# Kernel optimization log

Measured on AMD Instinct MI355X. Metric: run time of the kernel, lower is better.

The kernel has to match this reference:

```python
import jax, jax.numpy as jnp
import numpy as np
import math

B, S, D, H = 1, 4096, 1024, 16
HD = D // H  # head_dim = 64


def setup_inputs() -> dict:
    key = jax.random.key(0)
    ks = jax.random.split(key, 6)
    x = jax.random.normal(ks[0], (B, S, D), dtype=jnp.float32)
    # Llama-style rotary frequencies: theta = 10000^{-2i/head_dim}
    inv_freq = 1.0 / (10000.0 ** (jnp.arange(0, HD, 2, dtype=jnp.float32) / HD))  # (HD/2,)
    t = jnp.arange(S, dtype=jnp.float32)
    freqs = jnp.outer(t, inv_freq)  # (S, HD/2)
    cos = jnp.cos(freqs)
    sin = jnp.sin(freqs)
    # additive causal mask (S, S): 0 on/below diagonal, -inf above
    mask = jnp.where(jnp.tril(jnp.ones((S, S), dtype=bool)), 0.0, -jnp.inf).astype(jnp.float32)
    scale = 1.0 / math.sqrt(D)
    wq = jax.random.normal(ks[1], (D, D), dtype=jnp.float32) * scale
    wk = jax.random.normal(ks[2], (D, D), dtype=jnp.float32) * scale
    wv = jax.random.normal(ks[3], (D, D), dtype=jnp.float32) * scale
    wo = jax.random.normal(ks[4], (D, D), dtype=jnp.float32) * scale
    return {"x": x, "cos": cos, "sin": sin, "mask": mask,
            "wq": wq, "wk": wk, "wv": wv, "wo": wo, "start_pos": 0}


def _rope(t, cos, sin):
    # t: (b, s, h, hd); cos/sin: (s, hd/2). Interleaved-pair complex rotation.
    b, s, h, hd = t.shape
    tr = t.reshape(b, s, h, hd // 2, 2)
    te, to = tr[..., 0], tr[..., 1]
    c = cos[None, :, None, :]
    sn = sin[None, :, None, :]
    oe = te * c - to * sn
    oo = te * sn + to * c
    return jnp.stack([oe, oo], axis=-1).reshape(b, s, h, hd)


def reference(x, cos, sin, mask, wq, wk, wv, wo, start_pos):
    b, s, d = x.shape
    h, hd = H, HD
    # Linear layers: y = x @ W.T (torch nn.Linear convention, W is (out,in))
    xq = (x @ wq.T).reshape(b, s, h, hd)
    xk = (x @ wk.T).reshape(b, s, h, hd)
    xv = (x @ wv.T).reshape(b, s, h, hd)
    xq = _rope(xq, cos, sin)
    xk = _rope(xk, cos, sin)
    # (b, h, s, hd)
    xq = xq.transpose(0, 2, 1, 3)
    xk = xk.transpose(0, 2, 1, 3)
    xv = xv.transpose(0, 2, 1, 3)
    scores = jnp.einsum('bhqd,bhkd->bhqk', xq, xk) / math.sqrt(hd)
    scores = scores + mask[None, None, :, :]
    attn = jax.nn.softmax(scores.astype(jnp.float32), axis=-1).astype(xq.dtype)
    out = jnp.einsum('bhqk,bhkd->bhqd', attn, xv)
    out = out.transpose(0, 2, 1, 3).reshape(b, s, d)
    return out @ wo.T
```

## Files before the change

### kernel.cpp

```cpp
#include <hip/hip_runtime.h>
#include <hip/hip_bf16.h>
#include <math.h>

typedef __bf16 bf16;
typedef __bf16 bf16x4 __attribute__((ext_vector_type(4)));
typedef __bf16 bf16x8 __attribute__((ext_vector_type(8)));
typedef float floatx4 __attribute__((ext_vector_type(4)));
typedef short short4v __attribute__((ext_vector_type(4)));

#define S_LEN 4096
#define DM 1024
#define NH 16
#define HD 64

#define GM 4096
#define GN 1024
#define GK 1024
#define FST 68

#define QSCALE 0.18033688011112042f

#define GLDS16(gp, lp) __builtin_amdgcn_global_load_lds( \
    (const __attribute__((address_space(1))) void*)(gp), \
    (__attribute__((address_space(3))) void*)(lp), 16, 0, 0)

__global__ void cvt_bf16(const float* __restrict__ x,  const float* __restrict__ wq,
                         const float* __restrict__ wk, const float* __restrict__ wv,
                         const float* __restrict__ wo, bf16* __restrict__ dst)
{
    size_t i4 = ((size_t)blockIdx.x * 256 + threadIdx.x) * 4;
    const float* src; size_t off;
    const size_t M1 = (size_t)1 << 20;
    if      (i4 < 4 * M1) { src = x;  off = i4;          }
    else if (i4 < 5 * M1) { src = wq; off = i4 - 4 * M1; }
    else if (i4 < 6 * M1) { src = wk; off = i4 - 5 * M1; }
    else if (i4 < 7 * M1) { src = wv; off = i4 - 6 * M1; }
    else                  { src = wo; off = i4 - 7 * M1; }
    float4 v = *(const float4*)(src + off);
    bf16x4 o = { (bf16)v.x, (bf16)v.y, (bf16)v.z, (bf16)v.w };
    *(bf16x4*)(&dst[i4]) = o;
}

__launch_bounds__(256)
__global__ void gemm_qkv(const bf16* __restrict__ A,
                         const bf16* __restrict__ B0, const bf16* __restrict__ B1,
                         const bf16* __restrict__ B2,
                         const float* __restrict__ cosp, const float* __restrict__ sinp,
                         bf16* __restrict__ Qw, bf16* __restrict__ Kw,
                         bf16* __restrict__ VTw)
{
    const int bid = blockIdx.x;
    const int swz = (bid & 7) * 192 + (bid >> 3);
    const int bz  = swz >> 9;
    const int rem = swz & 511;
    const int m0  = (rem >> 3) * 64;
    const int n0  = (rem & 7) * 128;
    const bf16* __restrict__ B = (bz == 0) ? B0 : (bz == 1 ? B1 : B2);

    const int tid  = threadIdx.x;
    const int wave = tid >> 6;
    const int lane = tid & 63;
    const int wm   = (wave >> 1) * 32;
    const int wn   = (wave & 1) * 64;
    const int lrow = lane >> 4;
    const int lcol = lane & 15;

    __shared__ __align__(16) bf16 As[64 * 64];
    __shared__ __align__(16) bf16 Bs[128 * 64];

    floatx4 acc[2][4];
    #pragma unroll
    for (int i = 0; i < 2; i++)
        #pragma unroll
        for (int j = 0; j < 4; j++) acc[i][j] = (floatx4){0.f, 0.f, 0.f, 0.f};

    const int swc = (((lane & 7) ^ ((lane >> 3) & 7))) * 8;
    const bf16* ga0 = A + (size_t)(m0 + wave * 16 + (lane >> 3)) * GK + swc;
    const bf16* gb0 = B + (size_t)(n0 + wave * 32 + (lane >> 3)) * GK + swc;
    bf16* la = &As[(wave * 16) * 64];
    bf16* lb = &Bs[(wave * 32) * 64];
    const int kof0 = ((0 + lrow) ^ (lcol & 7)) * 8;
    const int kof1 = ((4 + lrow) ^ (lcol & 7)) * 8;

    for (int kt = 0; kt < GK; kt += 64) {
        #pragma unroll
        for (int i = 0; i < 2; i++)
            GLDS16(ga0 + kt + (size_t)i * 8 * GK, la + i * 8 * 64);
        #pragma unroll
        for (int i = 0; i < 4; i++)
            GLDS16(gb0 + kt + (size_t)i * 8 * GK, lb + i * 8 * 64);
        __syncthreads();
        #pragma unroll
        for (int ks = 0; ks < 2; ks++) {
            const int ko = ks ? kof1 : kof0;
            bf16x8 af[2], bfr[4];
            #pragma unroll
            for (int t = 0; t < 2; t++)
                af[t]  = *(const bf16x8*)(&As[(wm + t * 16 + lcol) * 64 + ko]);
            #pragma unroll
            for (int t = 0; t < 4; t++)
                bfr[t] = *(const bf16x8*)(&Bs[(wn + t * 16 + lcol) * 64 + ko]);
            #pragma unroll
            for (int mt = 0; mt < 2; mt++)
                #pragma unroll
                for (int nt = 0; nt < 4; nt++)
                    acc[mt][nt] = __builtin_amdgcn_mfma_f32_16x16x32_bf16(af[mt], bfr[nt], acc[mt][nt], 0, 0, 0);
        }
        __syncthreads();
    }

    if (bz < 2) {
        bf16* __restrict__ C = bz ? Kw : Qw;
        const float qs = (bz == 0) ? QSCALE : 1.0f;
        const bool odd = (lcol & 1);
        #pragma unroll
        for (int mt = 0; mt < 2; mt++)
            #pragma unroll
            for (int nt = 0; nt < 4; nt++) {
                int i = (nt * 16 + lcol) >> 1;
                #pragma unroll
                for (int r = 0; r < 4; r++) {
                    float v  = acc[mt][nt][r];
                    float pv = __shfl_xor(v, 1, 64);
                    int s = m0 + wm + mt * 16 + lrow * 4 + r;
                    float c  = cosp[s * 32 + i];
                    float sn = sinp[s * 32 + i];
                    float ov = odd ? (pv * sn + v * c) : (v * c - pv * sn);
                    C[(size_t)s * GN + n0 + wn + nt * 16 + lcol] = (bf16)(ov * qs);
                }
            }
    } else {
        #pragma unroll
        for (int mt = 0; mt < 2; mt++)
            #pragma unroll
            for (int nt = 0; nt < 4; nt++) {
                int col = n0 + wn + nt * 16 + lcol;
                int s   = m0 + wm + mt * 16 + lrow * 4;
                bf16x4 ov = { (bf16)acc[mt][nt][0], (bf16)acc[mt][nt][1],
                              (bf16)acc[mt][nt][2], (bf16)acc[mt][nt][3] };
                *(bf16x4*)(&VTw[(size_t)col * S_LEN + s]) = ov;
            }
    }
}

__launch_bounds__(256, 4)
__global__ void flash_attn(const bf16* __restrict__ Q, const bf16* __restrict__ K,
                           const bf16* __restrict__ VT,
                           float* __restrict__ O0, float* __restrict__ O1,
                           float* __restrict__ L0, float* __restrict__ L1)
{
    const int h    = blockIdx.y;
    const int pi0  = blockIdx.x >> 1;
    const int pi   = ((h >> 2) & 1) ? (31 - pi0) : pi0;
    const int p    = blockIdx.x & 1;
    const int tid  = threadIdx.x;
    const int wave = tid >> 6;
    const int lane = tid & 63;
    const int lrow = lane >> 4;
    const int lcol = lane & 15;

    const int qtA = pi;
    const int qtB = 63 - pi;

    float* __restrict__ Op = p ? O1 : O0;
    float* __restrict__ Lp = p ? L1 : L0;

    __shared__ __align__(16) bf16 Ks[2][64 * FST];
    __shared__ __align__(16) bf16 Vs[2][64 * FST];

    const int q0A = qtA * 64 + wave * 16;
    const int q0B = qtB * 64 + wave * 16;

    const bf16* qpA = Q + (size_t)(q0A + lcol) * DM + h * HD;
    const bf16* qpB = Q + (size_t)(q0B + lcol) * DM + h * HD;
    bf16x8 qfA[2], qfB[2];
    qfA[0] = *(const bf16x8*)(qpA + 0 + lrow * 8);
    qfA[1] = *(const bf16x8*)(qpA + 32 + lrow * 8);
    qfB[0] = *(const bf16x8*)(qpB + 0 + lrow * 8);
    qfB[1] = *(const bf16x8*)(qpB + 32 + lrow * 8);

    float lA = 0.f, lB = 0.f;
    floatx4 oaccA[4], oaccB[4];
    #pragma unroll
    for (int nt = 0; nt < 4; nt++) {
        oaccA[nt] = (floatx4){0.f, 0.f, 0.f, 0.f};
        oaccB[nt] = (floatx4){0.f, 0.f, 0.f, 0.f};
    }

    const int  srow = tid >> 3;
    const int  sch  = (tid & 7) * 8;
    const bf16* kp  = K  + (size_t)srow * DM + h * HD + sch;
    const bf16* vp  = VT + (size_t)(h * HD + srow) * S_LEN + sch;
    const int  wof  = srow * FST + sch;

    {
        size_t ko = (size_t)p * 64 * DM;
        size_t vo = (size_t)p * 64;
        uint4 a = *(const uint4*)(kp + ko);
        uint4 b = *(const uint4*)(kp + ko + (size_t)32 * DM);
        uint4 c = *(const uint4*)(vp + vo);
        uint4 d = *(const uint4*)(vp + vo + (size_t)32 * S_LEN);
        *(uint4*)(&Ks[0][wof])            = a;
        *(uint4*)(&Ks[0][wof + 32 * FST]) = b;
        *(uint4*)(&Vs[0][wof])            = c;
        *(uint4*)(&Vs[0][wof + 32 * FST]) = d;
    }
    __syncthreads();

    uint4 kr0, kr1, vr0, vr1;
    for (int t = p; t <= qtB; t += 2) {
        const int  cur  = ((t - p) >> 1) & 1;
        const bool more = (t + 2 <= qtB);
        const bool actA = (t <= qtA);

        if (more) {
            size_t ko = (size_t)(t + 2) * 64 * DM;
            size_t vo = (size_t)(t + 2) * 64;
            kr0 = *(const uint4*)(kp + ko);
            kr1 = *(const uint4*)(kp + ko + (size_t)32 * DM);
            vr0 = *(const uint4*)(vp + vo);
            vr1 = *(const uint4*)(vp + vo + (size_t)32 * S_LEN);
        }

        short4v pbA[4], pbB[4];
        const bool diagA = (t == qtA);
        const bool diagB = (t == qtB);
        #pragma unroll
        for (int nt = 0; nt < 4; nt++) {
            floatx4 zB = (floatx4){0.f, 0.f, 0.f, 0.f};
            floatx4 zA = (floatx4){0.f, 0.f, 0.f, 0.f};
            __builtin_amdgcn_s_setprio(1);
            #pragma unroll
            for (int ks = 0; ks < 2; ks++) {
                bf16x8 kf = *(const bf16x8*)(&Ks[cur][(nt * 16 + lcol) * FST + ks * 32 + lrow * 8]);
                zB = __builtin_amdgcn_mfma_f32_16x16x32_bf16(kf, qfB[ks], zB, 0, 0, 0);
                if (actA)
                    zA = __builtin_amdgcn_mfma_f32_16x16x32_bf16(kf, qfA[ks], zA, 0, 0, 0);
            }
            __builtin_amdgcn_s_setprio(0);
            if (diagB) {
                #pragma unroll
                for (int r = 0; r < 4; r++) {
                    int kg = t * 64 + nt * 16 + lrow * 4 + r;
                    float pr = exp2f(zB[r]);
                    if (kg > q0B + lcol) pr = 0.f;
                    zB[r] = pr; lB += pr;
                }
            } else {
                #pragma unroll
                for (int r = 0; r < 4; r++) {
                    float pr = exp2f(zB[r]);
                    zB[r] = pr; lB += pr;
                }
            }
            bf16x4 pvB = { (bf16)zB[0], (bf16)zB[1], (bf16)zB[2], (bf16)zB[3] };
            pbB[nt] = __builtin_bit_cast(short4v, pvB);
            if (actA) {
                if (diagA) {
                    #pragma unroll
                    for (int r = 0; r < 4; r++) {
                        int kg = t * 64 + nt * 16 + lrow * 4 + r;
                        float pr = exp2f(zA[r]);
                        if (kg > q0A + lcol) pr = 0.f;
                        zA[r] = pr; lA += pr;
                    }
                } else {
                    #pragma unroll
                    for (int r = 0; r < 4; r++) {
                        float pr = exp2f(zA[r]);
                        zA[r] = pr; lA += pr;
                    }
                }
                bf16x4 pvA = { (bf16)zA[0], (bf16)zA[1], (bf16)zA[2], (bf16)zA[3] };
                pbA[nt] = __builtin_bit_cast(short4v, pvA);
            }
        }

        __builtin_amdgcn_s_setprio(1);
        #pragma unroll
        for (int nt = 0; nt < 4; nt++)
            #pragma unroll
            for (int kt = 0; kt < 4; kt++) {
                bf16x4 va = *(const bf16x4*)(&Vs[cur][(nt * 16 + lcol) * FST + kt * 16 + lrow * 4]);
                short4v vas = __builtin_bit_cast(short4v, va);
                oaccB[nt] = __builtin_amdgcn_mfma_f32_16x16x16bf16_1k(vas, pbB[kt], oaccB[nt], 0, 0, 0);
                if (actA)
                    oaccA[nt] = __builtin_amdgcn_mfma_f32_16x16x16bf16_1k(vas, pbA[kt], oaccA[nt], 0, 0, 0);
            }
        __builtin_amdgcn_s_setprio(0);

        if (more) {
            int nxt = cur ^ 1;
            *(uint4*)(&Ks[nxt][wof])            = kr0;
            *(uint4*)(&Ks[nxt][wof + 32 * FST]) = kr1;
            *(uint4*)(&Vs[nxt][wof])            = vr0;
            *(uint4*)(&Vs[nxt][wof + 32 * FST]) = vr1;
        }
        __syncthreads();
    }

    lA += __shfl_xor(lA, 16, 64);
    lA += __shfl_xor(lA, 32, 64);
    lB += __shfl_xor(lB, 16, 64);
    lB += __shfl_xor(lB, 32, 64);
    if (lrow == 0) {
        Lp[h * S_LEN + q0A + lcol] = lA;
        Lp[h * S_LEN + q0B + lcol] = lB;
    }
    #pragma unroll
    for (int nt = 0; nt < 4; nt++) {
        *(floatx4*)(&Op[(size_t)(q0A + lcol) * DM + h * HD + nt * 16 + lrow * 4]) = oaccA[nt];
        *(floatx4*)(&Op[(size_t)(q0B + lcol) * DM + h * HD + nt * 16 + lrow * 4]) = oaccB[nt];
    }
}

__global__ void combine_kernel(const float* __restrict__ O0, const float* __restrict__ O1,
                               const float* __restrict__ L0, const float* __restrict__ L1,
                               bf16* __restrict__ Aw)
{
    int i4 = (blockIdx.x * 256 + threadIdx.x) * 4;
    int q = i4 >> 10;
    int c = i4 & 1023;
    int h = c >> 6;
    float rl = 1.f / (L0[h * S_LEN + q] + L1[h * S_LEN + q]);
    float4 a = *(const float4*)(O0 + i4);
    float4 b = *(const float4*)(O1 + i4);
    bf16x4 o = { (bf16)((a.x + b.x) * rl), (bf16)((a.y + b.y) * rl),
                 (bf16)((a.z + b.z) * rl), (bf16)((a.w + b.w) * rl) };
    *(bf16x4*)(&Aw[i4]) = o;
}

__launch_bounds__(256)
__global__ void gemm_out(const bf16* __restrict__ A, const bf16* __restrict__ B,
                         float* __restrict__ out)
{
    const int bid = blockIdx.x;
    const int swz = (bid & 7) * 64 + (bid >> 3);
    const int m0  = (swz >> 3) * 64;
    const int n0  = (swz & 7) * 128;

    const int tid  = threadIdx.x;
    const int wave = tid >> 6;
    const int lane = tid & 63;
    const int wm   = (wave >> 1) * 32;
    const int wn   = (wave & 1) * 64;
    const int lrow = lane >> 4;
    const int lcol = lane & 15;

    __shared__ __align__(16) bf16 As[2][64 * 64];
    __shared__ __align__(16) bf16 Bs[2][128 * 64];

    floatx4 acc[2][4];
    #pragma unroll
    for (int i = 0; i < 2; i++)
        #pragma unroll
        for (int j = 0; j < 4; j++) acc[i][j] = (floatx4){0.f, 0.f, 0.f, 0.f};

    const int swc = (((lane & 7) ^ ((lane >> 3) & 7))) * 8;
    const bf16* ga0 = A + (size_t)(m0 + wave * 16 + (lane >> 3)) * GK + swc;
    const bf16* gb0 = B + (size_t)(n0 + wave * 32 + (lane >> 3)) * GK + swc;
    const int kof0 = ((0 + lrow) ^ (lcol & 7)) * 8;
    const int kof1 = ((4 + lrow) ^ (lcol & 7)) * 8;

    #pragma unroll
    for (int i = 0; i < 2; i++)
        GLDS16(ga0 + (size_t)i * 8 * GK, &As[0][(wave * 16 + i * 8) * 64]);
    #pragma unroll
    for (int i = 0; i < 4; i++)
        GLDS16(gb0 + (size_t)i * 8 * GK, &Bs[0][(wave * 32 + i * 8) * 64]);
    __syncthreads();

    int cur = 0;
    for (int kt = 0; kt < GK; kt += 64) {
        if (kt + 64 < GK) {
            #pragma unroll
            for (int i = 0; i < 2; i++)
                GLDS16(ga0 + kt + 64 + (size_t)i * 8 * GK, &As[cur ^ 1][(wave * 16 + i * 8) * 64]);
            #pragma unroll
            for (int i = 0; i < 4; i++)
                GLDS16(gb0 + kt + 64 + (size_t)i * 8 * GK, &Bs[cur ^ 1][(wave * 32 + i * 8) * 64]);
        }
        #pragma unroll
        for (int ks = 0; ks < 2; ks++) {
            const int ko = ks ? kof1 : kof0;
            bf16x8 af[2], bfr[4];
            #pragma unroll
            for (int t = 0; t < 2; t++)
                af[t]  = *(const bf16x8*)(&As[cur][(wm + t * 16 + lcol) * 64 + ko]);
            #pragma unroll
            for (int t = 0; t < 4; t++)
                bfr[t] = *(const bf16x8*)(&Bs[cur][(wn + t * 16 + lcol) * 64 + ko]);
            #pragma unroll
            for (int mt = 0; mt < 2; mt++)
                #pragma unroll
                for (int nt = 0; nt < 4; nt++)
                    acc[mt][nt] = __builtin_amdgcn_mfma_f32_16x16x32_bf16(af[mt], bfr[nt], acc[mt][nt], 0, 0, 0);
        }
        __syncthreads();
        cur ^= 1;
    }

    #pragma unroll
    for (int mt = 0; mt < 2; mt++)
        #pragma unroll
        for (int nt = 0; nt < 4; nt++)
            #pragma unroll
            for (int r = 0; r < 4; r++) {
                int row = m0 + wm + mt * 16 + lrow * 4 + r;
                int col = n0 + wn + nt * 16 + lcol;
                out[(size_t)row * GN + col] = acc[mt][nt][r];
            }
}

extern "C" void kernel_launch(void* const* d_in, const int* in_sizes, int n_in,
                              void* d_out, int out_size, void* d_ws, size_t ws_size,
                              hipStream_t stream) {
    const float* x    = (const float*)d_in[0];
    const float* cosp = (const float*)d_in[1];
    const float* sinp = (const float*)d_in[2];
    const float* wq   = (const float*)d_in[4];
    const float* wk   = (const float*)d_in[5];
    const float* wv   = (const float*)d_in[6];
    const float* wo   = (const float*)d_in[7];
    float* out = (float*)d_out;

    const size_t SD = (size_t)S_LEN * DM;
    const size_t DD = (size_t)DM * DM;
    bf16* xb  = (bf16*)d_ws;
    bf16* wqb = xb + SD;
    bf16* wkb = wqb + DD;
    bf16* wvb = wkb + DD;
    bf16* wob = wvb + DD;
    bf16* Qw  = wob + DD;
    bf16* Kw  = Qw + SD;
    bf16* VTw = Kw + SD;
    bf16* Aw  = VTw + SD;
    float* O0f = (float*)(Aw + SD);
    float* O1f = O0f + SD;
    float* L0f = O1f + SD;
    float* L1f = L0f + (size_t)S_LEN * NH;

    cvt_bf16<<<8192, 256, 0, stream>>>(x, wq, wk, wv, wo, xb);
    gemm_qkv<<<1536, 256, 0, stream>>>(
        xb, wqb, wkb, wvb, cosp, sinp, Qw, Kw, VTw);
    flash_attn<<<dim3(64, NH), 256, 0, stream>>>(Qw, Kw, VTw, O0f, O1f, L0f, L1f);
    combine_kernel<<<S_LEN * DM / 1024, 256, 0, stream>>>(O0f, O1f, L0f, L1f, Aw);
    gemm_out<<<512, 256, 0, stream>>>(Aw, wob, out);
}
```

Before: 276.8 us.

## Merge two query-tile pairs per 512-thread attention block to share K/V tiles

```diff
diff --git a/kernel.cpp b/kernel.cpp
--- a/kernel.cpp
+++ b/kernel.cpp
@@ -143,24 +143,28 @@
     }
 }
 
-__launch_bounds__(256, 4)
+__launch_bounds__(512, 4)
 __global__ void flash_attn(const bf16* __restrict__ Q, const bf16* __restrict__ K,
                            const bf16* __restrict__ VT,
                            float* __restrict__ O0, float* __restrict__ O1,
                            float* __restrict__ L0, float* __restrict__ L1)
 {
-    const int h    = blockIdx.y;
-    const int pi0  = blockIdx.x >> 1;
-    const int pi   = ((h >> 2) & 1) ? (31 - pi0) : pi0;
-    const int p    = blockIdx.x & 1;
+    const int h   = blockIdx.y;
+    const int a0  = blockIdx.x >> 1;
+    const int a   = ((h >> 3) & 1) ? (15 - a0) : a0;
+    const int p   = blockIdx.x & 1;
     const int tid  = threadIdx.x;
     const int wave = tid >> 6;
+    const int g    = wave >> 2;
+    const int w4   = wave & 3;
     const int lane = tid & 63;
     const int lrow = lane >> 4;
     const int lcol = lane & 15;
 
-    const int qtA = pi;
-    const int qtB = 63 - pi;
+    const int pi   = 2 * a + g;
+    const int qtA  = pi;
+    const int qtB  = 63 - pi;
+    const int tmax = 63 - 2 * a;
 
     float* __restrict__ Op = p ? O1 : O0;
     float* __restrict__ Lp = p ? L1 : L0;
@@ -168,8 +172,8 @@
     __shared__ __align__(16) bf16 Ks[2][64 * FST];
     __shared__ __align__(16) bf16 Vs[2][64 * FST];
 
-    const int q0A = qtA * 64 + wave * 16;
-    const int q0B = qtB * 64 + wave * 16;
+    const int q0A = qtA * 64 + w4 * 16;
+    const int q0B = qtB * 64 + w4 * 16;
 
     const bf16* qpA = Q + (size_t)(q0A + lcol) * DM + h * HD;
     const bf16* qpB = Q + (size_t)(q0B + lcol) * DM + h * HD;
@@ -194,107 +198,98 @@
     const int  wof  = srow * FST + sch;
 
     {
-        size_t ko = (size_t)p * 64 * DM;
-        size_t vo = (size_t)p * 64;
-        uint4 a = *(const uint4*)(kp + ko);
-        uint4 b = *(const uint4*)(kp + ko + (size_t)32 * DM);
-        uint4 c = *(const uint4*)(vp + vo);
-        uint4 d = *(const uint4*)(vp + vo + (size_t)32 * S_LEN);
-        *(uint4*)(&Ks[0][wof])            = a;
-        *(uint4*)(&Ks[0][wof + 32 * FST]) = b;
-        *(uint4*)(&Vs[0][wof])            = c;
-        *(uint4*)(&Vs[0][wof + 32 * FST]) = d;
+        uint4 ak = *(const uint4*)(kp + (size_t)p * 64 * DM);
+        uint4 av = *(const uint4*)(vp + (size_t)p * 64);
+        *(uint4*)(&Ks[0][wof]) = ak;
+        *(uint4*)(&Vs[0][wof]) = av;
     }
     __syncthreads();
 
-    uint4 kr0, kr1, vr0, vr1;
-    for (int t = p; t <= qtB; t += 2) {
+    uint4 kr0, vr0;
+    for (int t = p; t <= tmax; t += 2) {
         const int  cur  = ((t - p) >> 1) & 1;
-        const bool more = (t + 2 <= qtB);
+        const bool more = (t + 2 <= tmax);
+        const bool actB = (t <= qtB);
         const bool actA = (t <= qtA);
 
         if (more) {
-            size_t ko = (size_t)(t + 2) * 64 * DM;
-            size_t vo = (size_t)(t + 2) * 64;
-            kr0 = *(const uint4*)(kp + ko);
-            kr1 = *(const uint4*)(kp + ko + (size_t)32 * DM);
-            vr0 = *(const uint4*)(vp + vo);
-            vr1 = *(const uint4*)(vp + vo + (size_t)32 * S_LEN);
+            kr0 = *(const uint4*)(kp + (size_t)(t + 2) * 64 * DM);
+            vr0 = *(const uint4*)(vp + (size_t)(t + 2) * 64);
         }
 
         short4v pbA[4], pbB[4];
-        const bool diagA = (t == qtA);
-        const bool diagB = (t == qtB);
-        #pragma unroll
-        for (int nt = 0; nt < 4; nt++) {
-            floatx4 zB = (floatx4){0.f, 0.f, 0.f, 0.f};
-            floatx4 zA = (floatx4){0.f, 0.f, 0.f, 0.f};
-            __builtin_amdgcn_s_setprio(1);
-            #pragma unroll
-            for (int ks = 0; ks < 2; ks++) {
-                bf16x8 kf = *(const bf16x8*)(&Ks[cur][(nt * 16 + lcol) * FST + ks * 32 + lrow * 8]);
-                zB = __builtin_amdgcn_mfma_f32_16x16x32_bf16(kf, qfB[ks], zB, 0, 0, 0);
-                if (actA)
-                    zA = __builtin_amdgcn_mfma_f32_16x16x32_bf16(kf, qfA[ks], zA, 0, 0, 0);
-            }
-            __builtin_amdgcn_s_setprio(0);
-            if (diagB) {
+        if (actB) {
+            const bool diagA = (t == qtA);
+            const bool diagB = (t == qtB);
+            #pragma unroll
+            for (int nt = 0; nt < 4; nt++) {
+                floatx4 zB = (floatx4){0.f, 0.f, 0.f, 0.f};
+                floatx4 zA = (floatx4){0.f, 0.f, 0.f, 0.f};
+                __builtin_amdgcn_s_setprio(1);
                 #pragma unroll
-                for (int r = 0; r < 4; r++) {
-                    int kg = t * 64 + nt * 16 + lrow * 4 + r;
-                    float pr = exp2f(zB[r]);
-                    if (kg > q0B + lcol) pr = 0.f;
-                    zB[r] = pr; lB += pr;
+                for (int ks = 0; ks < 2; ks++) {
+                    bf16x8 kf = *(const bf16x8*)(&Ks[cur][(nt * 16 + lcol) * FST + ks * 32 + lrow * 8]);
+                    zB = __builtin_amdgcn_mfma_f32_16x16x32_bf16(kf, qfB[ks], zB, 0, 0, 0);
+                    if (actA)
+                        zA = __builtin_amdgcn_mfma_f32_16x16x32_bf16(kf, qfA[ks], zA, 0, 0, 0);
                 }
-            } else {
-                #pragma unroll
-                for (int r = 0; r < 4; r++) {
-                    float pr = exp2f(zB[r]);
-                    zB[r] = pr; lB += pr;
-                }
-            }
-            bf16x4 pvB = { (bf16)zB[0], (bf16)zB[1], (bf16)zB[2], (bf16)zB[3] };
-            pbB[nt] = __builtin_bit_cast(short4v, pvB);
-            if (actA) {
-                if (diagA) {
+                __builtin_amdgcn_s_setprio(0);
+                if (diagB) {
                     #pragma unroll
                     for (int r = 0; r < 4; r++) {
                         int kg = t * 64 + nt * 16 + lrow * 4 + r;
-                        float pr = exp2f(zA[r]);
-                        if (kg > q0A + lcol) pr = 0.f;
-                        zA[r] = pr; lA += pr;
+                        float pr = exp2f(zB[r]);
+                        if (kg > q0B + lcol) pr = 0.f;
+                        zB[r] = pr; lB += pr;
                     }
                 } else {
                     #pragma unroll
                     for (int r = 0; r < 4; r++) {
-                        float pr = exp2f(zA[r]);
-                        zA[r] = pr; lA += pr;
+                        float pr = exp2f(zB[r]);
+                        zB[r] = pr; lB += pr;
                     }
                 }
-                bf16x4 pvA = { (bf16)zA[0], (bf16)zA[1], (bf16)zA[2], (bf16)zA[3] };
-                pbA[nt] = __builtin_bit_cast(short4v, pvA);
+                bf16x4 pvB = { (bf16)zB[0], (bf16)zB[1], (bf16)zB[2], (bf16)zB[3] };
+                pbB[nt] = __builtin_bit_cast(short4v, pvB);
+                if (actA) {
+                    if (diagA) {
+                        #pragma unroll
+                        for (int r = 0; r < 4; r++) {
+                            int kg = t * 64 + nt * 16 + lrow * 4 + r;
+                            float pr = exp2f(zA[r]);
+                            if (kg > q0A + lcol) pr = 0.f;
+                            zA[r] = pr; lA += pr;
+                        }
+                    } else {
+                        #pragma unroll
+                        for (int r = 0; r < 4; r++) {
+                            float pr = exp2f(zA[r]);
+                            zA[r] = pr; lA += pr;
+                        }
+                    }
+                    bf16x4 pvA = { (bf16)zA[0], (bf16)zA[1], (bf16)zA[2], (bf16)zA[3] };
+                    pbA[nt] = __builtin_bit_cast(short4v, pvA);
+                }
             }
-        }
-
-        __builtin_amdgcn_s_setprio(1);
-        #pragma unroll
-        for (int nt = 0; nt < 4; nt++)
-            #pragma unroll
-            for (int kt = 0; kt < 4; kt++) {
-                bf16x4 va = *(const bf16x4*)(&Vs[cur][(nt * 16 + lcol) * FST + kt * 16 + lrow * 4]);
-                short4v vas = __builtin_bit_cast(short4v, va);
-                oaccB[nt] = __builtin_amdgcn_mfma_f32_16x16x16bf16_1k(vas, pbB[kt], oaccB[nt], 0, 0, 0);
-                if (actA)
-                    oaccA[nt] = __builtin_amdgcn_mfma_f32_16x16x16bf16_1k(vas, pbA[kt], oaccA[nt], 0, 0, 0);
-            }
-        __builtin_amdgcn_s_setprio(0);
+
+            __builtin_amdgcn_s_setprio(1);
+            #pragma unroll
+            for (int nt = 0; nt < 4; nt++)
+                #pragma unroll
+                for (int kt = 0; kt < 4; kt++) {
+                    bf16x4 va = *(const bf16x4*)(&Vs[cur][(nt * 16 + lcol) * FST + kt * 16 + lrow * 4]);
+                    short4v vas = __builtin_bit_cast(short4v, va);
+                    oaccB[nt] = __builtin_amdgcn_mfma_f32_16x16x16bf16_1k(vas, pbB[kt], oaccB[nt], 0, 0, 0);
+                    if (actA)
+                        oaccA[nt] = __builtin_amdgcn_mfma_f32_16x16x16bf16_1k(vas, pbA[kt], oaccA[nt], 0, 0, 0);
+                }
+            __builtin_amdgcn_s_setprio(0);
+        }
 
         if (more) {
             int nxt = cur ^ 1;
-            *(uint4*)(&Ks[nxt][wof])            = kr0;
-            *(uint4*)(&Ks[nxt][wof + 32 * FST]) = kr1;
-            *(uint4*)(&Vs[nxt][wof])            = vr0;
-            *(uint4*)(&Vs[nxt][wof + 32 * FST]) = vr1;
+            *(uint4*)(&Ks[nxt][wof]) = kr0;
+            *(uint4*)(&Vs[nxt][wof]) = vr0;
         }
         __syncthreads();
     }
@@ -443,7 +438,7 @@
     cvt_bf16<<<8192, 256, 0, stream>>>(x, wq, wk, wv, wo, xb);
     gemm_qkv<<<1536, 256, 0, stream>>>(
         xb, wqb, wkb, wvb, cosp, sinp, Qw, Kw, VTw);
-    flash_attn<<<dim3(64, NH), 256, 0, stream>>>(Qw, Kw, VTw, O0f, O1f, L0f, L1f);
+    flash_attn<<<dim3(32, NH), 512, 0, stream>>>(Qw, Kw, VTw, O0f, O1f, L0f, L1f);
     combine_kernel<<<S_LEN * DM / 1024, 256, 0, stream>>>(O0f, O1f, L0f, L1f, Aw);
     gemm_out<<<512, 256, 0, stream>>>(Aw, wob, out);
 }
```

After: 272.4 us. No clear change (-1.6%).
